# Kernel tuning notes

Hardware: AMD Instinct MI355X
Metric: run time of the kernel (lower is better)

Reference implementation:

```python
import jax, jax.numpy as jnp
import numpy as np

N, D_IN, UNITS = 8192, 4096, 4096

def setup_inputs() -> dict:
    key = jax.random.key(0)
    k1, k2 = jax.random.split(key)
    x = jax.random.normal(k1, (N, D_IN), dtype=jnp.float32)
    # weight initialized RandomNormal(stddev=0.1) in the original build()
    w = jax.random.normal(k2, (D_IN, UNITS), dtype=jnp.float32) * 0.1
    return {"x": x, "w": w}

def reference(x, w):
    # BinaryDense: sign-binarize both activations and weights, then dense matmul.
    # tf.sign semantics: sign(0) == 0, matched by jnp.sign.
    x_bin = jnp.sign(x)  # [N, d_in]
    w_bin = jnp.sign(w)  # [d_in, units]
    return jnp.matmul(x_bin, w_bin)  # [N, units]
```

## Files before the change

### kernel.cpp

```cpp
#include <hip/hip_runtime.h>
#include <stdint.h>

#define M_DIM 8192
#define K_DIM 4096
#define N_DIM 4096
#define KB (K_DIM / 2)

typedef unsigned char u8;
typedef unsigned int u32;
typedef int i32x4 __attribute__((ext_vector_type(4)));
typedef int i32x8 __attribute__((ext_vector_type(8)));
typedef float f32x4 __attribute__((ext_vector_type(4)));
typedef float float4v __attribute__((ext_vector_type(4)));
typedef u32 u32x2 __attribute__((ext_vector_type(2)));

__device__ __forceinline__ u32 sign_fp4(float v) {
  return v > 0.0f ? 0x2u : (v < 0.0f ? 0xAu : 0x0u);
}

__device__ __forceinline__ u32 pk16(u32 v) {
  return (v & 0xFu) | ((v >> 4) & 0xF0u) | ((v >> 8) & 0xF00u) | ((v >> 12) & 0xF000u);
}

__global__ void binarize_fused(const float* __restrict__ x, const float* __restrict__ w,
                               u32* __restrict__ xb, u8* __restrict__ wT) {
  const int tid = threadIdx.x;
  const int bid = blockIdx.x;
  const int r3 = bid % 3;
  if (r3 != 2) {
    __shared__ u8 tile[64][68];
    const int wtile = (bid / 3) * 2 + r3;
    const int bn = (wtile & 63) * 64;
    const int bk = (wtile >> 6) * 64;

#pragma unroll
    for (int it = 0; it < 4; ++it) {
      int idx = tid + it * 256;
      int rr = idx >> 4;
      int c = (idx & 15) * 4;
      float4v v = *(const float4v*)&w[(size_t)(bk + rr) * N_DIM + bn + c];
      tile[c + 0][rr] = (u8)sign_fp4(v.x);
      tile[c + 1][rr] = (u8)sign_fp4(v.y);
      tile[c + 2][rr] = (u8)sign_fp4(v.z);
      tile[c + 3][rr] = (u8)sign_fp4(v.w);
    }
    __syncthreads();
    const int rn = tid >> 2;
    const int cbyte = (tid & 3) * 8;
    const u32* trow = (const u32*)&tile[rn][0];
    u32 q0 = trow[cbyte / 2 + 0];
    u32 q1 = trow[cbyte / 2 + 1];
    u32 q2 = trow[cbyte / 2 + 2];
    u32 q3 = trow[cbyte / 2 + 3];
    u32x2 o;
    o.x = pk16(q0) | (pk16(q1) << 16);
    o.y = pk16(q2) | (pk16(q3) << 16);
    *(u32x2*)&wT[(size_t)(bn + rn) * KB + (bk >> 1) + cbyte] = o;
  } else {
    const int n8 = M_DIM * K_DIM / 8;
    int i = (bid / 3) * 256 + tid;
    const int stride = 2048 * 256;
    for (; i < n8; i += stride) {
      float4v v0 = ((const float4v*)x)[2 * i];
      float4v v1 = ((const float4v*)x)[2 * i + 1];
      u32 wd = sign_fp4(v0.x) | (sign_fp4(v0.y) << 4) | (sign_fp4(v0.z) << 8) |
               (sign_fp4(v0.w) << 12) | (sign_fp4(v1.x) << 16) | (sign_fp4(v1.y) << 20) |
               (sign_fp4(v1.z) << 24) | (sign_fp4(v1.w) << 28);
      xb[i] = wd;
    }
  }
}

#define BM 256
#define BN 256
#define BKB 128
#define NT (K_DIM / 256)

__device__ __forceinline__ void gload_lds16(const u8* g, u8* l) {
  __builtin_amdgcn_global_load_lds(
      (const __attribute__((address_space(1))) void*)g,
      (__attribute__((address_space(3))) void*)l, 16, 0, 0);
}

__device__ __forceinline__ i32x8 pad8(i32x4 v) {
  return __builtin_shufflevector(v, v, 0, 1, 2, 3, -1, -1, -1, -1);
}

__device__ __forceinline__ f32x4 mfma_fp4(i32x4 a, i32x4 b, f32x4 c) {
  return __builtin_amdgcn_mfma_scale_f32_16x16x128_f8f6f4(pad8(a), pad8(b), c, 4, 4, 0, 0x7F, 0,
                                                          0x7F);
}

__global__ __launch_bounds__(512, 2) void gemm_bin_fp4(const u8* __restrict__ Ag,
                                                       const u8* __restrict__ Btg,
                                                       float* __restrict__ C) {
  __shared__ u8 lds[2][4][128 * 128];

  const int tid = threadIdx.x;
  const int lane = tid & 63;
  const int wid = tid >> 6;
  const int wr = wid >> 2;
  const int wc = wid & 3;

  const int b = blockIdx.x;
  const int sw = (b & 7) * (gridDim.x >> 3) + (b >> 3);
  const int tiles_n = N_DIM / BN;
  const int bm = (sw / tiles_n) * BM;
  const int bn = (sw % tiles_n) * BN;

  const int l15 = lane & 15;
  const int g4 = lane >> 4;
  const int brow0 = (wc & 1) * 64;
  const int srow = lane >> 3;
  const int swz_src = (((lane & 7) ^ srow) << 4);

  auto stage = [&](int buf, int slot, const u8* gbase) {
#pragma unroll
    for (int i = 0; i < 2; ++i) {
      const u8* g = gbase + (size_t)(i * 64 + wid * 8 + srow) * KB + swz_src;
      gload_lds16(g, &lds[buf][slot][(i * 64 + wid * 8) * 128]);
    }
  };

  f32x4 acc[8][4] = {};

  {
    const u8* Abase = Ag + (size_t)bm * KB;
    const u8* Bbase = Btg + (size_t)bn * KB;
    stage(0, 0, Abase);
    stage(0, 1, Abase + (size_t)128 * KB);
    stage(0, 2, Bbase);
    stage(0, 3, Bbase + (size_t)128 * KB);
    stage(1, 2, Bbase + BKB);
    stage(1, 3, Bbase + (size_t)128 * KB + BKB);
  }
  asm volatile("s_waitcnt vmcnt(4)" ::: "memory");
  __builtin_amdgcn_s_barrier();

  i32x4 a0[4], b0[4];
  {
    const u8* As0 = &lds[0][wr][0];
    const u8* Bs0 = &lds[0][2 + (wc >> 1)][0];
#pragma unroll
    for (int m = 0; m < 4; ++m) {
      int row = m * 16 + l15;
      a0[m] = *(const i32x4*)&As0[row * 128 + ((g4 * 16) ^ ((row & 7) << 4))];
    }
#pragma unroll
    for (int n = 0; n < 4; ++n) {
      int row = brow0 + n * 16 + l15;
      b0[n] = *(const i32x4*)&Bs0[row * 128 + ((g4 * 16) ^ ((row & 7) << 4))];
    }
  }

  for (int t = 0; t < NT; ++t) {
    const int buf = t & 1;
    const u8* As = &lds[buf][wr][0];
    const u8* Bs = &lds[buf][2 + (wc >> 1)][0];
    const u8* AsN = &lds[buf ^ 1][wr][0];
    const u8* BsN = &lds[buf ^ 1][2 + (wc >> 1)][0];

    i32x4 a1[4], a2[4], a3[4], b1[4];

#pragma unroll
    for (int m = 0; m < 4; ++m) {
      int row = m * 16 + l15;
      a1[m] = *(const i32x4*)&As[row * 128 + ((64 + g4 * 16) ^ ((row & 7) << 4))];
    }
#pragma unroll
    for (int n = 0; n < 4; ++n) {
      int row = brow0 + n * 16 + l15;
      b1[n] = *(const i32x4*)&Bs[row * 128 + ((64 + g4 * 16) ^ ((row & 7) << 4))];
    }
    if (t + 1 < NT) {
      const u8* An = Ag + (size_t)bm * KB + (t + 1) * BKB;
      stage(buf ^ 1, 0, An);
      stage(buf ^ 1, 1, An + (size_t)128 * KB);
    }
    __builtin_amdgcn_sched_barrier(0);

    __builtin_amdgcn_s_setprio(1);
#pragma unroll
    for (int m = 0; m < 4; ++m)
#pragma unroll
      for (int n = 0; n < 4; ++n)
        acc[m][n] = mfma_fp4(a0[m], b0[n], acc[m][n]);
    __builtin_amdgcn_s_setprio(0);
    __builtin_amdgcn_sched_barrier(0);

#pragma unroll
    for (int m = 0; m < 4; ++m) {
      int row = 64 + m * 16 + l15;
      a2[m] = *(const i32x4*)&As[row * 128 + ((g4 * 16) ^ ((row & 7) << 4))];
    }
    __builtin_amdgcn_sched_barrier(0);

    __builtin_amdgcn_s_setprio(1);
#pragma unroll
    for (int m = 0; m < 4; ++m)
#pragma unroll
      for (int n = 0; n < 4; ++n)
        acc[m][n] = mfma_fp4(a1[m], b1[n], acc[m][n]);
    __builtin_amdgcn_s_setprio(0);

    asm volatile("s_waitcnt vmcnt(0)" ::: "memory");
    __builtin_amdgcn_s_barrier();

    if (t + 2 < NT) {
      const u8* Bn = Btg + (size_t)bn * KB + (t + 2) * BKB;
      stage(buf, 2, Bn);
      stage(buf, 3, Bn + (size_t)128 * KB);
    }
#pragma unroll
    for (int m = 0; m < 4; ++m) {
      int row = 64 + m * 16 + l15;
      a3[m] = *(const i32x4*)&As[row * 128 + ((64 + g4 * 16) ^ ((row & 7) << 4))];
    }
    __builtin_amdgcn_sched_barrier(0);

    __builtin_amdgcn_s_setprio(1);
#pragma unroll
    for (int m = 0; m < 4; ++m)
#pragma unroll
      for (int n = 0; n < 4; ++n)
        acc[4 + m][n] = mfma_fp4(a2[m], b0[n], acc[4 + m][n]);
    __builtin_amdgcn_s_setprio(0);
    __builtin_amdgcn_sched_barrier(0);

    if (t + 1 < NT) {
#pragma unroll
      for (int m = 0; m < 4; ++m) {
        int row = m * 16 + l15;
        a0[m] = *(const i32x4*)&AsN[row * 128 + ((g4 * 16) ^ ((row & 7) << 4))];
      }
#pragma unroll
      for (int n = 0; n < 4; ++n) {
        int row = brow0 + n * 16 + l15;
        b0[n] = *(const i32x4*)&BsN[row * 128 + ((g4 * 16) ^ ((row & 7) << 4))];
      }
    }
    __builtin_amdgcn_sched_barrier(0);

    __builtin_amdgcn_s_setprio(1);
#pragma unroll
    for (int m = 0; m < 4; ++m)
#pragma unroll
      for (int n = 0; n < 4; ++n)
        acc[4 + m][n] = mfma_fp4(a3[m], b1[n], acc[4 + m][n]);
    __builtin_amdgcn_s_setprio(0);

    __builtin_amdgcn_s_barrier();
  }

  const int crow0 = bm + wr * 128;
  const int ccol0 = bn + wc * 64;
#pragma unroll
  for (int m = 0; m < 8; ++m)
#pragma unroll
    for (int n = 0; n < 4; ++n)
#pragma unroll
      for (int j = 0; j < 4; ++j)
        C[(size_t)(crow0 + m * 16 + g4 * 4 + j) * N_DIM + ccol0 + n * 16 + l15] = acc[m][n][j];
}

__global__ void naive_bin_gemm(const float* __restrict__ X, const float* __restrict__ W,
                               float* __restrict__ C) {
  int j = blockIdx.x * blockDim.x + threadIdx.x;
  int i = blockIdx.y;
  if (j >= N_DIM) return;
  float s = 0.0f;
  for (int k = 0; k < K_DIM; ++k) {
    float xv = X[(size_t)i * K_DIM + k];
    float wv = W[(size_t)k * N_DIM + j];
    float sx = (float)((xv > 0.0f) - (xv < 0.0f));
    float sw = (float)((wv > 0.0f) - (wv < 0.0f));
    s += sx * sw;
  }
  C[(size_t)i * N_DIM + j] = s;
}

extern "C" void kernel_launch(void* const* d_in, const int* in_sizes, int n_in,
                              void* d_out, int out_size, void* d_ws, size_t ws_size,
                              hipStream_t stream) {
  const float* x = (const float*)d_in[0];
  const float* w = (const float*)d_in[1];
  float* out = (float*)d_out;

  const size_t xb_bytes = (size_t)M_DIM * KB;
  const size_t wt_bytes = (size_t)N_DIM * KB;

  if (ws_size >= xb_bytes + wt_bytes) {
    u8* xb = (u8*)d_ws;
    u8* wt = (u8*)((char*)d_ws + xb_bytes);

    binarize_fused<<<6144, 256, 0, stream>>>(x, w, (u32*)xb, wt);

    const int grid = (M_DIM / BM) * (N_DIM / BN);
    gemm_bin_fp4<<<grid, 512, 0, stream>>>(xb, wt, out);
  } else {
    naive_bin_gemm<<<dim3(N_DIM / 256, M_DIM), dim3(256), 0, stream>>>(x, w, out);
  }
}
```

Before: 125.7 us.

## Give alternating warps a mirrored sub-tile order to spread LDS bank traffic

Waves get a role from (wid>>2 ^ wid)&1. Role-1 waves run the four A sub-tile MFMA phases in the reverse order (rows 64-127 first), so at any moment half the waves read different LDS rows than the other half. The aim is to stagger LDS reads and MFMA bursts across waves and so reduce bank contention and issue collisions. Each role has its own full code branch, which adds code size, and the branch on role is uniform within a wave, so it should not diverge.

```diff
diff --git a/kernel.cpp b/kernel.cpp
--- a/kernel.cpp
+++ b/kernel.cpp
@@ -101,6 +101,7 @@
   const int wid = tid >> 6;
   const int wr = wid >> 2;
   const int wc = wid & 3;
+  const int role = ((wid >> 2) ^ wid) & 1;
 
   const int b = blockIdx.x;
   const int sw = (b & 7) * (gridDim.x >> 3) + (b >> 3);
@@ -137,14 +138,15 @@
   asm volatile("s_waitcnt vmcnt(4)" ::: "memory");
   __builtin_amdgcn_s_barrier();
 
-  i32x4 a0[4], b0[4];
+  i32x4 p0[4], b0[4];
   {
     const u8* As0 = &lds[0][wr][0];
     const u8* Bs0 = &lds[0][2 + (wc >> 1)][0];
+    const int prerow = role ? 64 : 0;
 #pragma unroll
     for (int m = 0; m < 4; ++m) {
-      int row = m * 16 + l15;
-      a0[m] = *(const i32x4*)&As0[row * 128 + ((g4 * 16) ^ ((row & 7) << 4))];
+      int row = prerow + m * 16 + l15;
+      p0[m] = *(const i32x4*)&As0[row * 128 + ((g4 * 16) ^ ((row & 7) << 4))];
     }
 #pragma unroll
     for (int n = 0; n < 4; ++n) {
@@ -159,95 +161,166 @@
     const u8* Bs = &lds[buf][2 + (wc >> 1)][0];
     const u8* AsN = &lds[buf ^ 1][wr][0];
     const u8* BsN = &lds[buf ^ 1][2 + (wc >> 1)][0];
-
-    i32x4 a1[4], a2[4], a3[4], b1[4];
-
-#pragma unroll
-    for (int m = 0; m < 4; ++m) {
-      int row = m * 16 + l15;
-      a1[m] = *(const i32x4*)&As[row * 128 + ((64 + g4 * 16) ^ ((row & 7) << 4))];
-    }
-#pragma unroll
-    for (int n = 0; n < 4; ++n) {
-      int row = brow0 + n * 16 + l15;
-      b1[n] = *(const i32x4*)&Bs[row * 128 + ((64 + g4 * 16) ^ ((row & 7) << 4))];
-    }
-    if (t + 1 < NT) {
-      const u8* An = Ag + (size_t)bm * KB + (t + 1) * BKB;
-      stage(buf ^ 1, 0, An);
-      stage(buf ^ 1, 1, An + (size_t)128 * KB);
-    }
-    __builtin_amdgcn_sched_barrier(0);
-
-    __builtin_amdgcn_s_setprio(1);
-#pragma unroll
-    for (int m = 0; m < 4; ++m)
-#pragma unroll
-      for (int n = 0; n < 4; ++n)
-        acc[m][n] = mfma_fp4(a0[m], b0[n], acc[m][n]);
-    __builtin_amdgcn_s_setprio(0);
-    __builtin_amdgcn_sched_barrier(0);
-
-#pragma unroll
-    for (int m = 0; m < 4; ++m) {
-      int row = 64 + m * 16 + l15;
-      a2[m] = *(const i32x4*)&As[row * 128 + ((g4 * 16) ^ ((row & 7) << 4))];
-    }
-    __builtin_amdgcn_sched_barrier(0);
-
-    __builtin_amdgcn_s_setprio(1);
-#pragma unroll
-    for (int m = 0; m < 4; ++m)
-#pragma unroll
-      for (int n = 0; n < 4; ++n)
-        acc[m][n] = mfma_fp4(a1[m], b1[n], acc[m][n]);
-    __builtin_amdgcn_s_setprio(0);
-
-    asm volatile("s_waitcnt vmcnt(0)" ::: "memory");
-    __builtin_amdgcn_s_barrier();
-
-    if (t + 2 < NT) {
-      const u8* Bn = Btg + (size_t)bn * KB + (t + 2) * BKB;
-      stage(buf, 2, Bn);
-      stage(buf, 3, Bn + (size_t)128 * KB);
-    }
-#pragma unroll
-    for (int m = 0; m < 4; ++m) {
-      int row = 64 + m * 16 + l15;
-      a3[m] = *(const i32x4*)&As[row * 128 + ((64 + g4 * 16) ^ ((row & 7) << 4))];
-    }
-    __builtin_amdgcn_sched_barrier(0);
-
-    __builtin_amdgcn_s_setprio(1);
-#pragma unroll
-    for (int m = 0; m < 4; ++m)
-#pragma unroll
-      for (int n = 0; n < 4; ++n)
-        acc[4 + m][n] = mfma_fp4(a2[m], b0[n], acc[4 + m][n]);
-    __builtin_amdgcn_s_setprio(0);
-    __builtin_amdgcn_sched_barrier(0);
-
-    if (t + 1 < NT) {
+    const u8* An = Ag + (size_t)bm * KB + (t + 1) * BKB;
+    const u8* Bn = Btg + (size_t)bn * KB + (t + 2) * BKB;
+
+    if (role == 0) {
+      i32x4 a1[4], a2[4], a3[4], b1[4];
 #pragma unroll
       for (int m = 0; m < 4; ++m) {
         int row = m * 16 + l15;
-        a0[m] = *(const i32x4*)&AsN[row * 128 + ((g4 * 16) ^ ((row & 7) << 4))];
+        a1[m] = *(const i32x4*)&As[row * 128 + ((64 + g4 * 16) ^ ((row & 7) << 4))];
       }
 #pragma unroll
       for (int n = 0; n < 4; ++n) {
         int row = brow0 + n * 16 + l15;
-        b0[n] = *(const i32x4*)&BsN[row * 128 + ((g4 * 16) ^ ((row & 7) << 4))];
-      }
-    }
-    __builtin_amdgcn_sched_barrier(0);
-
-    __builtin_amdgcn_s_setprio(1);
-#pragma unroll
-    for (int m = 0; m < 4; ++m)
-#pragma unroll
-      for (int n = 0; n < 4; ++n)
-        acc[4 + m][n] = mfma_fp4(a3[m], b1[n], acc[4 + m][n]);
-    __builtin_amdgcn_s_setprio(0);
+        b1[n] = *(const i32x4*)&Bs[row * 128 + ((64 + g4 * 16) ^ ((row & 7) << 4))];
+      }
+      if (t + 1 < NT) {
+        stage(buf ^ 1, 0, An);
+        stage(buf ^ 1, 1, An + (size_t)128 * KB);
+      }
+      __builtin_amdgcn_sched_barrier(0);
+      __builtin_amdgcn_s_setprio(1);
+#pragma unroll
+      for (int m = 0; m < 4; ++m)
+#pragma unroll
+        for (int n = 0; n < 4; ++n)
+          acc[m][n] = mfma_fp4(p0[m], b0[n], acc[m][n]);
+      __builtin_amdgcn_s_setprio(0);
+      __builtin_amdgcn_sched_barrier(0);
+#pragma unroll
+      for (int m = 0; m < 4; ++m) {
+        int row = 64 + m * 16 + l15;
+        a2[m] = *(const i32x4*)&As[row * 128 + ((g4 * 16) ^ ((row & 7) << 4))];
+      }
+      __builtin_amdgcn_sched_barrier(0);
+      __builtin_amdgcn_s_setprio(1);
+#pragma unroll
+      for (int m = 0; m < 4; ++m)
+#pragma unroll
+        for (int n = 0; n < 4; ++n)
+          acc[m][n] = mfma_fp4(a1[m], b1[n], acc[m][n]);
+      __builtin_amdgcn_s_setprio(0);
+      asm volatile("s_waitcnt vmcnt(0)" ::: "memory");
+      __builtin_amdgcn_s_barrier();
+      if (t + 2 < NT) {
+        stage(buf, 2, Bn);
+        stage(buf, 3, Bn + (size_t)128 * KB);
+      }
+#pragma unroll
+      for (int m = 0; m < 4; ++m) {
+        int row = 64 + m * 16 + l15;
+        a3[m] = *(const i32x4*)&As[row * 128 + ((64 + g4 * 16) ^ ((row & 7) << 4))];
+      }
+      __builtin_amdgcn_sched_barrier(0);
+      __builtin_amdgcn_s_setprio(1);
+#pragma unroll
+      for (int m = 0; m < 4; ++m)
+#pragma unroll
+        for (int n = 0; n < 4; ++n)
+          acc[4 + m][n] = mfma_fp4(a2[m], b0[n], acc[4 + m][n]);
+      __builtin_amdgcn_s_setprio(0);
+      __builtin_amdgcn_sched_barrier(0);
+      if (t + 1 < NT) {
+#pragma unroll
+        for (int m = 0; m < 4; ++m) {
+          int row = m * 16 + l15;
+          p0[m] = *(const i32x4*)&AsN[row * 128 + ((g4 * 16) ^ ((row & 7) << 4))];
+        }
+#pragma unroll
+        for (int n = 0; n < 4; ++n) {
+          int row = brow0 + n * 16 + l15;
+          b0[n] = *(const i32x4*)&BsN[row * 128 + ((g4 * 16) ^ ((row & 7) << 4))];
+        }
+      }
+      __builtin_amdgcn_sched_barrier(0);
+      __builtin_amdgcn_s_setprio(1);
+#pragma unroll
+      for (int m = 0; m < 4; ++m)
+#pragma unroll
+        for (int n = 0; n < 4; ++n)
+          acc[4 + m][n] = mfma_fp4(a3[m], b1[n], acc[4 + m][n]);
+      __builtin_amdgcn_s_setprio(0);
+    } else {
+      i32x4 a3[4], b1[4], a0[4], a1[4];
+#pragma unroll
+      for (int m = 0; m < 4; ++m) {
+        int row = 64 + m * 16 + l15;
+        a3[m] = *(const i32x4*)&As[row * 128 + ((64 + g4 * 16) ^ ((row & 7) << 4))];
+      }
+#pragma unroll
+      for (int n = 0; n < 4; ++n) {
+        int row = brow0 + n * 16 + l15;
+        b1[n] = *(const i32x4*)&Bs[row * 128 + ((64 + g4 * 16) ^ ((row & 7) << 4))];
+      }
+      if (t + 1 < NT) {
+        stage(buf ^ 1, 0, An);
+        stage(buf ^ 1, 1, An + (size_t)128 * KB);
+      }
+      __builtin_amdgcn_sched_barrier(0);
+      __builtin_amdgcn_s_setprio(1);
+#pragma unroll
+      for (int m = 0; m < 4; ++m)
+#pragma unroll
+        for (int n = 0; n < 4; ++n)
+          acc[4 + m][n] = mfma_fp4(p0[m], b0[n], acc[4 + m][n]);
+      __builtin_amdgcn_s_setprio(0);
+      __builtin_amdgcn_sched_barrier(0);
+#pragma unroll
+      for (int m = 0; m < 4; ++m) {
+        int row = m * 16 + l15;
+        a0[m] = *(const i32x4*)&As[row * 128 + ((g4 * 16) ^ ((row & 7) << 4))];
+      }
+      __builtin_amdgcn_sched_barrier(0);
+      __builtin_amdgcn_s_setprio(1);
+#pragma unroll
+      for (int m = 0; m < 4; ++m)
+#pragma unroll
+        for (int n = 0; n < 4; ++n)
+          acc[4 + m][n] = mfma_fp4(a3[m], b1[n], acc[4 + m][n]);
+      __builtin_amdgcn_s_setprio(0);
+      asm volatile("s_waitcnt vmcnt(0)" ::: "memory");
+      __builtin_amdgcn_s_barrier();
+      if (t + 2 < NT) {
+        stage(buf, 2, Bn);
+        stage(buf, 3, Bn + (size_t)128 * KB);
+      }
+#pragma unroll
+      for (int m = 0; m < 4; ++m) {
+        int row = m * 16 + l15;
+        a1[m] = *(const i32x4*)&As[row * 128 + ((64 + g4 * 16) ^ ((row & 7) << 4))];
+      }
+      __builtin_amdgcn_sched_barrier(0);
+      __builtin_amdgcn_s_setprio(1);
+#pragma unroll
+      for (int m = 0; m < 4; ++m)
+#pragma unroll
+        for (int n = 0; n < 4; ++n)
+          acc[m][n] = mfma_fp4(a0[m], b0[n], acc[m][n]);
+      __builtin_amdgcn_s_setprio(0);
+      __builtin_amdgcn_sched_barrier(0);
+      if (t + 1 < NT) {
+#pragma unroll
+        for (int m = 0; m < 4; ++m) {
+          int row = 64 + m * 16 + l15;
+          p0[m] = *(const i32x4*)&AsN[row * 128 + ((g4 * 16) ^ ((row & 7) << 4))];
+        }
+#pragma unroll
+        for (int n = 0; n < 4; ++n) {
+          int row = brow0 + n * 16 + l15;
+          b0[n] = *(const i32x4*)&BsN[row * 128 + ((g4 * 16) ^ ((row & 7) << 4))];
+        }
+      }
+      __builtin_amdgcn_sched_barrier(0);
+      __builtin_amdgcn_s_setprio(1);
+#pragma unroll
+      for (int m = 0; m < 4; ++m)
+#pragma unroll
+        for (int n = 0; n < 4; ++n)
+          acc[m][n] = mfma_fp4(a1[m], b1[n], acc[m][n]);
+      __builtin_amdgcn_s_setprio(0);
+    }
 
     __builtin_amdgcn_s_barrier();
   }
```

Result: slower. 175.5 us (+39.6%).
